# Kernel optimization log

Hardware: AMD Instinct MI355X
Metric: run time of the kernel (lower is better)

## Reference

```python
import jax, jax.numpy as jnp
import numpy as np

B, N, C, H = 2, 2048, 1024, 16
D = C // H
SCALE = 1.0 / np.sqrt(D)
MASK_VAL = -10000.0


def setup_inputs() -> dict:
    key = jax.random.key(0)
    k1, k2, k3 = jax.random.split(key, 3)
    hidden_state = jax.random.normal(k1, (B, N, C), dtype=jnp.float32)
    attention_mask = jax.random.randint(k2, (B, N), 0, 2) == 1  # True = padded
    # fused QKV projection weight, torch Linear convention: y = x @ W.T, W: [3C, C]
    W = jax.random.normal(k3, (3 * C, C), dtype=jnp.float32) * 0.02
    return {"hidden_state": hidden_state, "W": W, "attention_mask": attention_mask}


def reference(hidden_state, W, attention_mask):
    b, n, c = hidden_state.shape
    # fused QKV: [B,N,3C] -> [B,N,3,H,D] -> [3,B,H,N,D]
    wx = jnp.einsum('bnc,oc->bno', hidden_state, W).reshape(b, n, 3, H, D)
    wx = jnp.transpose(wx, (2, 0, 3, 1, 4))
    q, k, v = wx[0], wx[1], wx[2]
    scores = jnp.einsum('bhid,bhjd->bhij', q, k) * SCALE
    # construct_mask: pairwise OR of per-token padding mask, broadcast over heads
    m = attention_mask
    expanded = (m[:, None, :, None] | m[:, None, None, :])  # [B,1,N,N]
    scores = jnp.where(expanded, MASK_VAL, scores)
    scores = scores - jnp.max(scores, axis=-1, keepdims=True)
    att_weights = jax.nn.softmax(scores, axis=-1)
    # dropout_rate = 0.0 -> identity
    att = jnp.einsum('bhij,bhjd->bhid', att_weights, v)
    att = jnp.transpose(att, (0, 2, 1, 3)).reshape(b, n, c)
    return (att, att_weights)
```

## Files before the change

kernel.cpp:

```cpp
#include <hip/hip_runtime.h>


typedef unsigned short u16;
typedef __attribute__((ext_vector_type(8))) short bf16x8;
typedef __attribute__((ext_vector_type(4))) float f32x4;

#define B_ 2
#define N_ 2048
#define H_ 16
#define D_ 64
#define QKV_MAT 4194304
#define ATTW_OFF 4194304
#define OFF_MASK 25165824
#define OFF_FLAG 25182208
#define OFF_XB   25182464
#define OFF_WB   33571072

#define SCALE_L2 0.18033688011112042f
#define MASK_L2  -14426.950408889634f

__device__ __forceinline__ u16 f32_bf16(float f) {
  unsigned u = __float_as_uint(f);
  u += 0x7fffu + ((u >> 16) & 1u);
  return (u16)(u >> 16);
}
__device__ __forceinline__ float bf16_f32(unsigned h) {
  return __uint_as_float(h << 16);
}
__device__ __forceinline__ bf16x8 ld_frag(const u16* p) { return *(const bf16x8*)p; }

__device__ __forceinline__ void gld16(u16* l, const u16* g) {
  __builtin_amdgcn_global_load_lds(
      (const __attribute__((address_space(1))) void*)g,
      (__attribute__((address_space(3))) void*)l, 16, 0, 0);
}

__global__ void detect_prep(const unsigned char* __restrict__ mraw,
                            const unsigned* __restrict__ X32,
                            int* __restrict__ flag) {
  __shared__ int votes, mflags;
  const int tid = threadIdx.x;
  if (tid == 0) { votes = 0; mflags = 0; }
  __syncthreads();
  int v = 0;
  for (int i = tid; i < 4096; i += 256) {
    unsigned low = X32[i] & 0xFFFFu;
    unsigned e = (low >> 7) & 0xFFu;
    if (low == 0 || (e >= 80 && e <= 150)) v++;
  }
  atomicAdd(&votes, v);
  int fl = 0;
  for (int p = tid; p < B_ * N_; p += 256) {
    unsigned char c = mraw[p];
    if (c > 1) fl |= 1;
    if (c && (p & 3) == 1) fl |= 4;
    if (c && (p & 3) != 0) fl |= 2;
    if (c && (p & 7) == 4) fl |= 8;
  }
  if (fl) atomicOr(&mflags, fl);
  __syncthreads();
  if (tid == 0) { flag[0] = (votes < 2600) ? 1 : 0; flag[1] = mflags; }
}

__global__ __launch_bounds__(256) void convert_in(const void* __restrict__ X,
                                                  const void* __restrict__ W,
                                                  const unsigned char* __restrict__ mraw,
                                                  u16* __restrict__ Xb, u16* __restrict__ Wb,
                                                  int* __restrict__ mout,
                                                  const int* __restrict__ flag) {
  const int f32m = flag[0];
  const int f = flag[1];
  const int gid = blockIdx.x * 256 + threadIdx.x;
  for (int i = gid; i < B_ * N_; i += gridDim.x * 256) {
    int m;
    if (f & 1) {
      if (f & 4) m = (((const u16*)mraw)[i] & 0x7FFFu) != 0;
      else       m = (((const unsigned*)mraw)[i] << 1) != 0;
    } else if (f & 2) m = mraw[i] != 0;
    else if (f & 8)   m = ((const int*)mraw)[i] != 0;
    else              m = ((const long long*)mraw)[i] != 0;
    mout[i] = m;
  }
  const int XC = (B_ * N_ * 1024) / 8;
  const int WC = (3072 * 1024) / 8;
  for (int idx = gid; idx < XC + WC; idx += gridDim.x * 256) {
    const void* src; u16* dst; int c;
    if (idx < XC) { c = idx; src = X; dst = Xb; }
    else          { c = idx - XC; src = W; dst = Wb; }
    if (f32m) {
      const float4* s = (const float4*)src;
      float4 a = s[c * 2], b = s[c * 2 + 1];
      unsigned p0 = (unsigned)f32_bf16(a.x) | ((unsigned)f32_bf16(a.y) << 16);
      unsigned p1 = (unsigned)f32_bf16(a.z) | ((unsigned)f32_bf16(a.w) << 16);
      unsigned p2 = (unsigned)f32_bf16(b.x) | ((unsigned)f32_bf16(b.y) << 16);
      unsigned p3 = (unsigned)f32_bf16(b.z) | ((unsigned)f32_bf16(b.w) << 16);
      ((uint4*)dst)[c] = make_uint4(p0, p1, p2, p3);
    } else {
      ((uint4*)dst)[c] = ((const uint4*)src)[c];
    }
  }
}

__global__ __launch_bounds__(256) void qkv_gemm(const u16* __restrict__ X,
                                                const u16* __restrict__ W,
                                                u16* __restrict__ qkv) {
  __shared__ u16 xs[128 * 64];
  __shared__ u16 wsh[128 * 64];
  const int tid = threadIdx.x;
  const int w = tid >> 6, l = tid & 63, quad = l >> 4, ln = l & 15;
  const int r0 = blockIdx.y * 128;
  const int o0 = blockIdx.x * 128;

  const f32x4 z4 = {0.f, 0.f, 0.f, 0.f};
  f32x4 acc[2][8];
#pragma unroll
  for (int rt = 0; rt < 2; rt++)
#pragma unroll
    for (int ct = 0; ct < 8; ct++) acc[rt][ct] = z4;

  for (int kc = 0; kc < 1024; kc += 64) {
#pragma unroll
    for (int ro = 0; ro < 4; ro++) {
      int q = ro * 256 + tid;
      int r = q >> 3, s = q & 7;
      int c = s ^ (r & 7);
      gld16(xs + q * 8, X + (size_t)(r0 + r) * 1024 + kc + c * 8);
      gld16(wsh + q * 8, W + (size_t)(o0 + r) * 1024 + kc + c * 8);
    }
    __syncthreads();
#pragma unroll
    for (int k2 = 0; k2 < 2; k2++) {
      bf16x8 af[2], bfr[8];
#pragma unroll
      for (int rt = 0; rt < 2; rt++) {
        int row = w * 32 + rt * 16 + ln;
        int slot = (k2 * 4 + quad) ^ (row & 7);
        af[rt] = ld_frag(xs + row * 64 + slot * 8);
      }
#pragma unroll
      for (int ct = 0; ct < 8; ct++) {
        int row = ct * 16 + ln;
        int slot = (k2 * 4 + quad) ^ (row & 7);
        bfr[ct] = ld_frag(wsh + row * 64 + slot * 8);
      }
#pragma unroll
      for (int rt = 0; rt < 2; rt++)
#pragma unroll
        for (int ct = 0; ct < 8; ct++)
          acc[rt][ct] = __builtin_amdgcn_mfma_f32_16x16x32_bf16(af[rt], bfr[ct], acc[rt][ct], 0, 0, 0);
    }
    __syncthreads();
  }

  const int b = r0 >> 11;
#pragma unroll
  for (int rt = 0; rt < 2; rt++) {
#pragma unroll
    for (int ct = 0; ct < 8; ct++) {
      int o = o0 + ct * 16 + ln;
      int sel = o >> 10;
      int h = (o >> 6) & 15;
      int d = o & 63;
      int nbase = (r0 & 2047) + w * 32 + rt * 16 + quad * 4;
      if (sel < 2) {
        size_t base = (size_t)sel * QKV_MAT + ((size_t)(b * 16 + h) * N_ + nbase) * D_ + d;
#pragma unroll
        for (int g = 0; g < 4; g++)
          qkv[base + (size_t)g * D_] = f32_bf16(acc[rt][ct][g]);
      } else {
        size_t base = 2 * (size_t)QKV_MAT + ((size_t)(b * 16 + h) * D_ + d) * N_ + nbase;
        unsigned lo = (unsigned)f32_bf16(acc[rt][ct][0]) | ((unsigned)f32_bf16(acc[rt][ct][1]) << 16);
        unsigned hi = (unsigned)f32_bf16(acc[rt][ct][2]) | ((unsigned)f32_bf16(acc[rt][ct][3]) << 16);
        *(uint2*)(qkv + base) = make_uint2(lo, hi);
      }
    }
  }
}

__global__ __launch_bounds__(256) void attn_kernel(const u16* __restrict__ qkv,
                                                   const int* __restrict__ mask,
                                                   void* __restrict__ outv,
                                                   const int* __restrict__ flag) {
  __shared__ u16 qs[128 * 64];
  __shared__ u16 ks[64 * 64];
  __shared__ u16 vs[64 * 64];
  __shared__ u16 ps[128 * 72];
  __shared__ float mrow[128];
  __shared__ float rlrow[128];

  const int of32 = flag[0];
  u16* outh = (u16*)outv;
  float* outf = (float*)outv;

  const int tid = threadIdx.x;
  const int w = tid >> 6, l = tid & 63, quad = l >> 4, ln = l & 15;
  const int bh = blockIdx.x & 31;
  const int qt = blockIdx.x >> 5;
  const int b = bh >> 4, h = bh & 15;
  const int q0 = qt * 128;

  const u16* Qg = qkv + ((size_t)bh * N_ + q0) * D_;
  const u16* Kg = qkv + QKV_MAT + (size_t)bh * N_ * D_;
  const u16* Vg = qkv + 2 * (size_t)QKV_MAT + (size_t)bh * D_ * N_;
  const int* mb = mask + b * N_;
  const size_t attw_base = (size_t)ATTW_OFF + (size_t)bh * N_ * N_ + (size_t)q0 * N_;

#pragma unroll
  for (int ro = 0; ro < 4; ro++) {
    int q = ro * 256 + tid;
    int r = q >> 3, s = q & 7;
    int c = s ^ (r & 7);
    gld16(qs + q * 8, Qg + (size_t)r * D_ + c * 8);
  }
  int rowpad[2][4];
#pragma unroll
  for (int rt = 0; rt < 2; rt++)
#pragma unroll
    for (int g = 0; g < 4; g++)
      rowpad[rt][g] = mb[q0 + w * 32 + rt * 16 + quad * 4 + g];
  __syncthreads();

  bf16x8 qa[2][2];
#pragma unroll
  for (int rt = 0; rt < 2; rt++)
#pragma unroll
    for (int k2 = 0; k2 < 2; k2++) {
      int row = w * 32 + rt * 16 + ln;
      int slot = (k2 * 4 + quad) ^ (row & 7);
      qa[rt][k2] = ld_frag(qs + row * 64 + slot * 8);
    }

  float lsum[2][4] = {{0.f, 0.f, 0.f, 0.f}, {0.f, 0.f, 0.f, 0.f}};
  const f32x4 z4 = {0.f, 0.f, 0.f, 0.f};

  for (int kt = 0; kt < 32; kt++) {
#pragma unroll
    for (int ro = 0; ro < 2; ro++) {
      int q = ro * 256 + tid;
      int r = q >> 3, s = q & 7;
      int c = s ^ (r & 7);
      gld16(ks + q * 8, Kg + (size_t)(kt * 64 + r) * D_ + c * 8);
    }
    int cp[4];
#pragma unroll
    for (int ct = 0; ct < 4; ct++) cp[ct] = mb[kt * 64 + ct * 16 + ln];
    __syncthreads();

    f32x4 sacc[2][4];
#pragma unroll
    for (int rt = 0; rt < 2; rt++)
#pragma unroll
      for (int ct = 0; ct < 4; ct++) sacc[rt][ct] = z4;
#pragma unroll
    for (int k2 = 0; k2 < 2; k2++) {
      bf16x8 kb[4];
#pragma unroll
      for (int ct = 0; ct < 4; ct++) {
        int row = ct * 16 + ln;
        int slot = (k2 * 4 + quad) ^ (row & 7);
        kb[ct] = ld_frag(ks + row * 64 + slot * 8);
      }
#pragma unroll
      for (int rt = 0; rt < 2; rt++)
#pragma unroll
        for (int ct = 0; ct < 4; ct++)
          sacc[rt][ct] = __builtin_amdgcn_mfma_f32_16x16x32_bf16(qa[rt][k2], kb[ct], sacc[rt][ct], 0, 0, 0);
    }
    __syncthreads();
#pragma unroll
    for (int rt = 0; rt < 2; rt++)
#pragma unroll
      for (int g = 0; g < 4; g++) {
        float e = 0.f;
#pragma unroll
        for (int ct = 0; ct < 4; ct++) {
          float sv = sacc[rt][ct][g] * SCALE_L2;
          sv = (rowpad[rt][g] | cp[ct]) ? MASK_L2 : sv;
          e += __builtin_amdgcn_exp2f(sv);
        }
        lsum[rt][g] += e;
      }
  }

#pragma unroll
  for (int rt = 0; rt < 2; rt++)
#pragma unroll
    for (int g = 0; g < 4; g++) {
      float lv = lsum[rt][g];
      lv += __shfl_xor(lv, 1);
      lv += __shfl_xor(lv, 2);
      lv += __shfl_xor(lv, 4);
      lv += __shfl_xor(lv, 8);
      if (ln == 0) {
        int i = w * 32 + rt * 16 + quad * 4 + g;
        mrow[i] = rowpad[rt][g] ? MASK_L2 : 0.f;
        rlrow[i] = rowpad[rt][g] ? (1.f / 2048.f) : (1.f / lv);
      }
    }
  __syncthreads();

  bf16x8 qb[8][2];
  float mi[8], rli[8];
#pragma unroll
  for (int it = 0; it < 8; it++) {
    int row = it * 16 + ln;
#pragma unroll
    for (int k2 = 0; k2 < 2; k2++) {
      int slot = (k2 * 4 + quad) ^ (row & 7);
      qb[it][k2] = ld_frag(qs + row * 64 + slot * 8);
    }
    mi[it] = mrow[row];
    rli[it] = rlrow[row];
  }

  f32x4 oacc[2][4];
#pragma unroll
  for (int rt = 0; rt < 2; rt++)
#pragma unroll
    for (int dt = 0; dt < 4; dt++) oacc[rt][dt] = z4;

  for (int kt = 0; kt < 32; kt++) {
    __syncthreads();
#pragma unroll
    for (int ro = 0; ro < 2; ro++) {
      int q = ro * 256 + tid;
      int r = q >> 3, s = q & 7;
      int c = s ^ (r & 7);
      gld16(ks + q * 8, Kg + (size_t)(kt * 64 + r) * D_ + c * 8);
      gld16(vs + q * 8, Vg + (size_t)r * N_ + kt * 64 + c * 8);
    }
    int cpj[4];
#pragma unroll
    for (int g = 0; g < 4; g++) cpj[g] = mb[kt * 64 + w * 16 + quad * 4 + g];
    __syncthreads();

    bf16x8 ka[2];
#pragma unroll
    for (int k2 = 0; k2 < 2; k2++) {
      int row = w * 16 + ln;
      int slot = (k2 * 4 + quad) ^ (row & 7);
      ka[k2] = ld_frag(ks + row * 64 + slot * 8);
    }
#pragma unroll
    for (int it = 0; it < 8; it++) {
      f32x4 st = z4;
      st = __builtin_amdgcn_mfma_f32_16x16x32_bf16(ka[0], qb[it][0], st, 0, 0, 0);
      st = __builtin_amdgcn_mfma_f32_16x16x32_bf16(ka[1], qb[it][1], st, 0, 0, 0);
      bool rp = mi[it] < -5000.f;
      unsigned pk[4];
#pragma unroll
      for (int g = 0; g < 4; g++) {
        float sv = st[g] * SCALE_L2;
        sv = (cpj[g] || rp) ? MASK_L2 : sv;
        float p = __builtin_amdgcn_exp2f(sv - mi[it]) * rli[it];
        pk[g] = f32_bf16(p);
      }
      int iRow = it * 16 + ln;
      int jc = w * 16 + quad * 4;
      *(uint2*)(ps + iRow * 72 + jc) = make_uint2(pk[0] | (pk[1] << 16), pk[2] | (pk[3] << 16));
    }
    __syncthreads();

    if (!of32) {
#pragma unroll
      for (int ro = 0; ro < 4; ro++) {
        int q = ro * 256 + tid;
        int r = q >> 3, c = q & 7;
        uint4 v = *(const uint4*)(ps + r * 72 + c * 8);
        *(uint4*)(outh + attw_base + (size_t)r * N_ + kt * 64 + c * 8) = v;
      }
    } else {
#pragma unroll
      for (int ro = 0; ro < 8; ro++) {
        int q = ro * 256 + tid;
        int r = q >> 4, c4 = q & 15;
        uint2 v = *(const uint2*)(ps + r * 72 + c4 * 4);
        float4 o = make_float4(bf16_f32(v.x & 0xFFFFu), bf16_f32(v.x >> 16),
                               bf16_f32(v.y & 0xFFFFu), bf16_f32(v.y >> 16));
        *(float4*)(outf + attw_base + (size_t)r * N_ + kt * 64 + c4 * 4) = o;
      }
    }
#pragma unroll
    for (int k2 = 0; k2 < 2; k2++) {
      bf16x8 pa[2], vb[4];
#pragma unroll
      for (int rt = 0; rt < 2; rt++) {
        int row = w * 32 + rt * 16 + ln;
        pa[rt] = ld_frag(ps + row * 72 + k2 * 32 + quad * 8);
      }
#pragma unroll
      for (int dt = 0; dt < 4; dt++) {
        int row = dt * 16 + ln;
        int slot = (k2 * 4 + quad) ^ (row & 7);
        vb[dt] = ld_frag(vs + row * 64 + slot * 8);
      }
#pragma unroll
      for (int rt = 0; rt < 2; rt++)
#pragma unroll
        for (int dt = 0; dt < 4; dt++)
          oacc[rt][dt] = __builtin_amdgcn_mfma_f32_16x16x32_bf16(pa[rt], vb[dt], oacc[rt][dt], 0, 0, 0);
    }
  }

#pragma unroll
  for (int rt = 0; rt < 2; rt++)
#pragma unroll
    for (int dt = 0; dt < 4; dt++) {
      int d = dt * 16 + ln;
#pragma unroll
      for (int g = 0; g < 4; g++) {
        int i = w * 32 + rt * 16 + quad * 4 + g;
        size_t off = (size_t)(b * N_ + q0 + i) * 1024 + h * 64 + d;
        if (!of32) outh[off] = f32_bf16(oacc[rt][dt][g]);
        else       outf[off] = oacc[rt][dt][g];
      }
    }
}

extern "C" void kernel_launch(void* const* d_in, const int* in_sizes, int n_in,
                              void* d_out, int out_size, void* d_ws, size_t ws_size,
                              hipStream_t stream) {
  (void)in_sizes; (void)n_in; (void)out_size; (void)ws_size;
  const unsigned char* mraw = (const unsigned char*)d_in[2];
  char* ws = (char*)d_ws;
  u16* qkvws = (u16*)ws;
  int* maskws = (int*)(ws + OFF_MASK);
  int* flagws = (int*)(ws + OFF_FLAG);
  u16* Xb = (u16*)(ws + OFF_XB);
  u16* Wb = (u16*)(ws + OFF_WB);

  detect_prep<<<1, 256, 0, stream>>>(mraw, (const unsigned*)d_in[0], flagws);
  convert_in<<<1792, 256, 0, stream>>>(d_in[0], d_in[1], mraw, Xb, Wb, maskws, flagws);
  qkv_gemm<<<dim3(24, 32), 256, 0, stream>>>(Xb, Wb, qkvws);
  attn_kernel<<<512, 256, 0, stream>>>(qkvws, maskws, d_out, flagws);
}
```

Before: 713.4 us.

## Double-buffer K/V tiles in attention and widen detect_prep block

The attention kernel now keeps two shared-memory buffers each for the K and V tiles. The load of the next tile is issued before computing on the current one, in both the row-sum pass and the output pass, which removes one barrier per iteration. The goal is to hide global-to-LDS load latency behind MFMA and exp work, at the cost of extra LDS use that may lower occupancy. The detect_prep prologue kernel also launches 1024 threads instead of 256, with matching loop strides.

```diff
diff --git a/kernel.cpp b/kernel.cpp
--- a/kernel.cpp
+++ b/kernel.cpp
@@ -43,14 +43,14 @@
   if (tid == 0) { votes = 0; mflags = 0; }
   __syncthreads();
   int v = 0;
-  for (int i = tid; i < 4096; i += 256) {
+  for (int i = tid; i < 4096; i += 1024) {
     unsigned low = X32[i] & 0xFFFFu;
     unsigned e = (low >> 7) & 0xFFu;
     if (low == 0 || (e >= 80 && e <= 150)) v++;
   }
   atomicAdd(&votes, v);
   int fl = 0;
-  for (int p = tid; p < B_ * N_; p += 256) {
+  for (int p = tid; p < B_ * N_; p += 1024) {
     unsigned char c = mraw[p];
     if (c > 1) fl |= 1;
     if (c && (p & 3) == 1) fl |= 4;
@@ -182,8 +182,8 @@
                                                    void* __restrict__ outv,
                                                    const int* __restrict__ flag) {
   __shared__ u16 qs[128 * 64];
-  __shared__ u16 ks[64 * 64];
-  __shared__ u16 vs[64 * 64];
+  __shared__ u16 ks[2][64 * 64];
+  __shared__ u16 vs[2][64 * 64];
   __shared__ u16 ps[128 * 72];
   __shared__ float mrow[128];
   __shared__ float rlrow[128];
@@ -212,6 +212,13 @@
     int c = s ^ (r & 7);
     gld16(qs + q * 8, Qg + (size_t)r * D_ + c * 8);
   }
+#pragma unroll
+  for (int ro = 0; ro < 2; ro++) {
+    int q = ro * 256 + tid;
+    int r = q >> 3, s = q & 7;
+    int c = s ^ (r & 7);
+    gld16(ks[0] + q * 8, Kg + (size_t)r * D_ + c * 8);
+  }
   int rowpad[2][4];
 #pragma unroll
   for (int rt = 0; rt < 2; rt++)
@@ -234,17 +241,19 @@
   const f32x4 z4 = {0.f, 0.f, 0.f, 0.f};
 
   for (int kt = 0; kt < 32; kt++) {
-#pragma unroll
-    for (int ro = 0; ro < 2; ro++) {
-      int q = ro * 256 + tid;
-      int r = q >> 3, s = q & 7;
-      int c = s ^ (r & 7);
-      gld16(ks + q * 8, Kg + (size_t)(kt * 64 + r) * D_ + c * 8);
+    const int cur = kt & 1;
+    if (kt < 31) {
+#pragma unroll
+      for (int ro = 0; ro < 2; ro++) {
+        int q = ro * 256 + tid;
+        int r = q >> 3, s = q & 7;
+        int c = s ^ (r & 7);
+        gld16(ks[cur ^ 1] + q * 8, Kg + (size_t)((kt + 1) * 64 + r) * D_ + c * 8);
+      }
     }
     int cp[4];
 #pragma unroll
     for (int ct = 0; ct < 4; ct++) cp[ct] = mb[kt * 64 + ct * 16 + ln];
-    __syncthreads();
 
     f32x4 sacc[2][4];
 #pragma unroll
@@ -258,7 +267,7 @@
       for (int ct = 0; ct < 4; ct++) {
         int row = ct * 16 + ln;
         int slot = (k2 * 4 + quad) ^ (row & 7);
-        kb[ct] = ld_frag(ks + row * 64 + slot * 8);
+        kb[ct] = ld_frag(ks[cur] + row * 64 + slot * 8);
       }
 #pragma unroll
       for (int rt = 0; rt < 2; rt++)
@@ -266,7 +275,6 @@
         for (int ct = 0; ct < 4; ct++)
           sacc[rt][ct] = __builtin_amdgcn_mfma_f32_16x16x32_bf16(qa[rt][k2], kb[ct], sacc[rt][ct], 0, 0, 0);
     }
-    __syncthreads();
 #pragma unroll
     for (int rt = 0; rt < 2; rt++)
 #pragma unroll
@@ -280,6 +288,16 @@
         }
         lsum[rt][g] += e;
       }
+    __syncthreads();
+  }
+
+#pragma unroll
+  for (int ro = 0; ro < 2; ro++) {
+    int q = ro * 256 + tid;
+    int r = q >> 3, s = q & 7;
+    int c = s ^ (r & 7);
+    gld16(ks[0] + q * 8, Kg + (size_t)r * D_ + c * 8);
+    gld16(vs[0] + q * 8, Vg + (size_t)r * N_ + c * 8);
   }
 
 #pragma unroll
@@ -320,26 +338,17 @@
     for (int dt = 0; dt < 4; dt++) oacc[rt][dt] = z4;
 
   for (int kt = 0; kt < 32; kt++) {
-    __syncthreads();
-#pragma unroll
-    for (int ro = 0; ro < 2; ro++) {
-      int q = ro * 256 + tid;
-      int r = q >> 3, s = q & 7;
-      int c = s ^ (r & 7);
-      gld16(ks + q * 8, Kg + (size_t)(kt * 64 + r) * D_ + c * 8);
-      gld16(vs + q * 8, Vg + (size_t)r * N_ + kt * 64 + c * 8);
-    }
+    const int cur = kt & 1;
     int cpj[4];
 #pragma unroll
     for (int g = 0; g < 4; g++) cpj[g] = mb[kt * 64 + w * 16 + quad * 4 + g];
-    __syncthreads();
 
     bf16x8 ka[2];
 #pragma unroll
     for (int k2 = 0; k2 < 2; k2++) {
       int row = w * 16 + ln;
       int slot = (k2 * 4 + quad) ^ (row & 7);
-      ka[k2] = ld_frag(ks + row * 64 + slot * 8);
+      ka[k2] = ld_frag(ks[cur] + row * 64 + slot * 8);
     }
 #pragma unroll
     for (int it = 0; it < 8; it++) {
@@ -360,6 +369,17 @@
       *(uint2*)(ps + iRow * 72 + jc) = make_uint2(pk[0] | (pk[1] << 16), pk[2] | (pk[3] << 16));
     }
     __syncthreads();
+
+    if (kt < 31) {
+#pragma unroll
+      for (int ro = 0; ro < 2; ro++) {
+        int q = ro * 256 + tid;
+        int r = q >> 3, s = q & 7;
+        int c = s ^ (r & 7);
+        gld16(ks[cur ^ 1] + q * 8, Kg + (size_t)((kt + 1) * 64 + r) * D_ + c * 8);
+        gld16(vs[cur ^ 1] + q * 8, Vg + (size_t)r * N_ + (kt + 1) * 64 + c * 8);
+      }
+    }
 
     if (!of32) {
 #pragma unroll
@@ -392,7 +412,7 @@
       for (int dt = 0; dt < 4; dt++) {
         int row = dt * 16 + ln;
         int slot = (k2 * 4 + quad) ^ (row & 7);
-        vb[dt] = ld_frag(vs + row * 64 + slot * 8);
+        vb[dt] = ld_frag(vs[cur] + row * 64 + slot * 8);
       }
 #pragma unroll
       for (int rt = 0; rt < 2; rt++)
@@ -400,6 +420,7 @@
         for (int dt = 0; dt < 4; dt++)
           oacc[rt][dt] = __builtin_amdgcn_mfma_f32_16x16x32_bf16(pa[rt], vb[dt], oacc[rt][dt], 0, 0, 0);
     }
+    __syncthreads();
   }
 
 #pragma unroll
@@ -429,7 +450,7 @@
   u16* Xb = (u16*)(ws + OFF_XB);
   u16* Wb = (u16*)(ws + OFF_WB);
 
-  detect_prep<<<1, 256, 0, stream>>>(mraw, (const unsigned*)d_in[0], flagws);
+  detect_prep<<<1, 1024, 0, stream>>>(mraw, (const unsigned*)d_in[0], flagws);
   convert_in<<<1792, 256, 0, stream>>>(d_in[0], d_in[1], mraw, Xb, Wb, maskws, flagws);
   qkv_gemm<<<dim3(24, 32), 256, 0, stream>>>(Xb, Wb, qkvws);
   attn_kernel<<<512, 256, 0, stream>>>(qkvws, maskws, d_out, flagws);
```

Result: faster. 690.4 us (-3.2%).
